# Kernel tuning notes

Measured on AMD Instinct MI355X. Metric: run time of the kernel, lower is better.

## Reference

```python
import jax, jax.numpy as jnp
import numpy as np

D = 1024
N_A = 4096
N_V = 4096


def setup_inputs() -> dict:
    key = jax.random.key(0)
    ks = jax.random.split(key, 6)
    s = 1.0 / np.sqrt(D)  # like torch Linear default init scale
    return {
        "inputs_a": jax.random.normal(ks[0], (N_A, D), dtype=jnp.float32),
        "inputs_v": jax.random.normal(ks[1], (N_V, D), dtype=jnp.float32),
        "W_Ba": jax.random.uniform(ks[2], (D, D), jnp.float32, -s, s),
        "W_Aa": jax.random.uniform(ks[3], (D, D), jnp.float32, -s, s),
        "W_Bv": jax.random.uniform(ks[4], (D, D), jnp.float32, -s, s),
        "W_Av": jax.random.uniform(ks[5], (D, D), jnp.float32, -s, s),
    }


def reference(inputs_a, inputs_v, W_Ba, W_Aa, W_Bv, W_Av):
    # torch Linear: y = x @ W.T ; weights stored [out, in]
    a_a = inputs_a @ W_Aa.T                      # [N_a, D]
    b_a = inputs_a @ W_Ba.T                      # [N_a, D]
    a_v = inputs_v @ W_Av.T                      # [N_v, D]
    b_v = inputs_v @ W_Bv.T                      # [N_v, D]
    scores = b_a @ a_v.T                         # [N_a, N_v]
    alpha_av = jax.nn.softmax(scores, axis=1)    # softmax over N_v
    att_avv = alpha_av @ b_v                     # [N_a, D]
    att_vaa = alpha_av.T @ a_a                   # [N_v, D]
    feature_map_a = att_avv + inputs_a
    feature_map_v = att_vaa + inputs_v
    return feature_map_a, feature_map_v
```

## Files before the change

### kernel.cpp

```cpp
#include <hip/hip_runtime.h>
#include <stdint.h>

#define D_DIM 1024
#define NA_DIM 4096
#define NV_DIM 4096

typedef __bf16 bf16_t;
typedef __bf16 bf16x8 __attribute__((ext_vector_type(8)));
typedef float f32x4 __attribute__((ext_vector_type(4)));

__device__ __forceinline__ void gload_lds16(const void* g, void* lds) {
  __builtin_amdgcn_global_load_lds(
      (const __attribute__((address_space(1))) unsigned int*)g,
      (__attribute__((address_space(3))) unsigned int*)lds, 16, 0, 0);
}

#define VMW(N) asm volatile("s_waitcnt vmcnt(" #N ")" ::: "memory")
#define LKW(N) asm volatile("s_waitcnt lgkmcnt(" #N ")" ::: "memory")
#define SB0() __builtin_amdgcn_sched_barrier(0)
#define BAR() asm volatile("s_barrier" ::: "memory")

__device__ __forceinline__ void gemm256_8ph(const bf16_t* __restrict__ A,
                                            const bf16_t* __restrict__ B,
                                            int K, int kb, int klen, int bm, int bn,
                                            bf16_t* lds, f32x4 acc[8][4]) {
  const int tid = threadIdx.x;
  const int lane = tid & 63;
  const int wid = tid >> 6;
  const int wm = wid >> 2;
  const int wn = wid & 3;
  const int frow = lane & 15;
  const int hi = lane >> 4;
  const int k0e = ((hi ^ (frow & 7)) << 3);

  const int sr = (wid << 4) + (lane >> 3);
  const int sc = (((lane & 7) ^ (lane >> 3)) << 3);
  const bf16_t* pAs = A + (size_t)(bm + sr) * K + kb + sc;
  const bf16_t* pBs = B + (size_t)(bn + sr) * K + kb + sc;
  const int dstW = wid << 10;

  const int aBase = (wm << 13) + frow * 64 + k0e;
  const int bBase = 16384 + ((wn >> 1) << 13) + ((wn & 1) << 12) + frow * 64 + k0e;

#define STG_A(kt, h, bufb) do { \
    const bf16_t* s_ = pAs + (size_t)((h) * 128) * K + (size_t)(kt) * 64; \
    bf16_t* d_ = lds + (bufb) * 32768 + (h) * 8192 + dstW; \
    gload_lds16(s_, d_); gload_lds16(s_ + (size_t)8 * K, d_ + 512); } while (0)
#define STG_B(kt, h, bufb) do { \
    const bf16_t* s_ = pBs + (size_t)((h) * 128) * K + (size_t)(kt) * 64; \
    bf16_t* d_ = lds + (bufb) * 32768 + 16384 + (h) * 8192 + dstW; \
    gload_lds16(s_, d_); gload_lds16(s_ + (size_t)8 * K, d_ + 512); } while (0)

  bf16x8 aF[2][4];
  bf16x8 bF[2][4][2];

#define READ_A(S, BUFB, Q) do { const bf16_t* Lb_ = lds + (BUFB) * 32768; \
    aF[S][0] = *(const bf16x8*)&Lb_[aBase + (Q) * 2048]; \
    aF[S][1] = *(const bf16x8*)&Lb_[(aBase ^ 32) + (Q) * 2048]; \
    aF[S][2] = *(const bf16x8*)&Lb_[aBase + (Q) * 2048 + 1024]; \
    aF[S][3] = *(const bf16x8*)&Lb_[(aBase ^ 32) + (Q) * 2048 + 1024]; } while (0)
#define READ_B(S, BUFB) do { const bf16_t* Lb_ = lds + (BUFB) * 32768; \
    _Pragma("unroll") for (int fc = 0; fc < 4; ++fc) { \
      bF[S][fc][0] = *(const bf16x8*)&Lb_[bBase + fc * 1024]; \
      bF[S][fc][1] = *(const bf16x8*)&Lb_[(bBase ^ 32) + fc * 1024]; } } while (0)

#define MFMA16(AS, BS, Q) do { \
    __builtin_amdgcn_s_setprio(1); \
    _Pragma("unroll") for (int fc = 0; fc < 4; ++fc) { \
      acc[(Q) * 2][fc]     = __builtin_amdgcn_mfma_f32_16x16x32_bf16(aF[AS][0], bF[BS][fc][0], acc[(Q) * 2][fc], 0, 0, 0); \
      acc[(Q) * 2][fc]     = __builtin_amdgcn_mfma_f32_16x16x32_bf16(aF[AS][1], bF[BS][fc][1], acc[(Q) * 2][fc], 0, 0, 0); \
      acc[(Q) * 2 + 1][fc] = __builtin_amdgcn_mfma_f32_16x16x32_bf16(aF[AS][2], bF[BS][fc][0], acc[(Q) * 2 + 1][fc], 0, 0, 0); \
      acc[(Q) * 2 + 1][fc] = __builtin_amdgcn_mfma_f32_16x16x32_bf16(aF[AS][3], bF[BS][fc][1], acc[(Q) * 2 + 1][fc], 0, 0, 0); \
    } \
    __builtin_amdgcn_s_setprio(0); } while (0)

  const int NI = klen >> 7;

  STG_B(0, 0, 0); STG_B(0, 1, 0); STG_A(0, 0, 0); STG_A(0, 1, 0);
  STG_B(1, 0, 1); STG_B(1, 1, 1);
  VMW(4);
  BAR();
  READ_B(0, 0); READ_A(0, 0, 0);

  for (int it = 0; it < NI; ++it) {
    const int T = 2 * it;
    const bool more = (it + 1 < NI);
    BAR(); STG_A(T + 1, 0, 1); READ_A(1, 0, 1); LKW(4); SB0(); MFMA16(0, 0, 0);
    BAR(); STG_A(T + 1, 1, 1); READ_A(0, 0, 2); LKW(4); SB0(); MFMA16(1, 0, 1);
    BAR(); if (more) STG_B(T + 2, 0, 0); READ_A(1, 0, 3); LKW(4); SB0(); MFMA16(0, 0, 2);
    BAR(); if (more) { STG_B(T + 2, 1, 0); VMW(4); } else { VMW(0); }
    READ_B(1, 1); READ_A(0, 1, 0); LKW(12); SB0(); MFMA16(1, 0, 3);
    BAR(); if (more) STG_A(T + 2, 0, 0); READ_A(1, 1, 1); LKW(4); SB0(); MFMA16(0, 1, 0);
    BAR(); if (more) STG_A(T + 2, 1, 0); READ_A(0, 1, 2); LKW(4); SB0(); MFMA16(1, 1, 1);
    BAR(); if (more) STG_B(T + 3, 0, 1); READ_A(1, 1, 3); LKW(4); SB0(); MFMA16(0, 1, 2);
    BAR();
    if (more) { STG_B(T + 3, 1, 1); VMW(4); READ_B(0, 0); READ_A(0, 0, 0); LKW(12); }
    else { LKW(0); }
    SB0(); MFMA16(1, 1, 3);
  }
#undef MFMA16
#undef READ_A
#undef READ_B
#undef STG_A
#undef STG_B
}

template <int BF16OUT>
__device__ __forceinline__ void store256(void* Cv, int ldc, int bm, int bn, f32x4 acc[8][4]) {
  const int lane = threadIdx.x & 63;
  const int wid = threadIdx.x >> 6;
  const int wm = wid >> 2, wn = wid & 3;
  const int frow = lane & 15, hi = lane >> 4;
  const int row0 = bm + wm * 128 + hi * 4;
  const int col0 = bn + wn * 64 + frow;
#pragma unroll
  for (int rf = 0; rf < 8; ++rf)
#pragma unroll
    for (int fc = 0; fc < 4; ++fc)
#pragma unroll
      for (int r = 0; r < 4; ++r) {
        size_t idx = (size_t)(row0 + rf * 16 + r) * ldc + (col0 + fc * 16);
        if constexpr (BF16OUT) ((bf16_t*)Cv)[idx] = (bf16_t)acc[rf][fc][r];
        else ((float*)Cv)[idx] = acc[rf][fc][r];
      }
}

__global__ __launch_bounds__(512, 2) void gemm_proj4(
    const bf16_t* __restrict__ Xa, const bf16_t* __restrict__ Xv,
    const bf16_t* __restrict__ W0, const bf16_t* __restrict__ W1,
    const bf16_t* __restrict__ W2, const bf16_t* __restrict__ W3,
    bf16_t* __restrict__ C0, bf16_t* __restrict__ C1,
    bf16_t* __restrict__ C2, bf16_t* __restrict__ C3) {
  __shared__ bf16_t lds[65536];
  const int z = blockIdx.z;
  const bf16_t* A = (z < 2) ? Xa : Xv;
  const bf16_t* B = (z == 0) ? W0 : (z == 1) ? W1 : (z == 2) ? W2 : W3;
  bf16_t* C = (z == 0) ? C0 : (z == 1) ? C1 : (z == 2) ? C2 : C3;
  f32x4 acc[8][4] = {};
  gemm256_8ph(A, B, D_DIM, 0, D_DIM, blockIdx.x * 256, blockIdx.y * 256, lds, acc);
  store256<1>(C, D_DIM, blockIdx.x * 256, blockIdx.y * 256, acc);
}

__global__ __launch_bounds__(512, 2) void gemm_scores(const bf16_t* __restrict__ A,
                                                      const bf16_t* __restrict__ B,
                                                      float* __restrict__ C) {
  __shared__ bf16_t lds[65536];
  f32x4 acc[8][4] = {};
  gemm256_8ph(A, B, D_DIM, 0, D_DIM, blockIdx.x * 256, blockIdx.y * 256, lds, acc);
  store256<0>(C, NV_DIM, blockIdx.x * 256, blockIdx.y * 256, acc);
}

__global__ __launch_bounds__(512, 2) void gemm_splitk(
    const bf16_t* __restrict__ alpha, const bf16_t* __restrict__ bvT,
    const bf16_t* __restrict__ alphaT, const bf16_t* __restrict__ aaT,
    float* __restrict__ P) {
  __shared__ bf16_t lds[65536];
  const int z = blockIdx.z;
  const bf16_t* A = (z < 2) ? alpha : alphaT;
  const bf16_t* B = (z < 2) ? bvT : aaT;
  const int kb = (z & 1) * 2048;
  f32x4 acc[8][4] = {};
  gemm256_8ph(A, B, 4096, kb, 2048, blockIdx.x * 256, blockIdx.y * 256, lds, acc);
  store256<0>(P + (size_t)z * NA_DIM * D_DIM, D_DIM, blockIdx.x * 256, blockIdx.y * 256, acc);
}

__global__ __launch_bounds__(256) void reduce_splitk(const float* __restrict__ P,
                                                     const float* __restrict__ resA,
                                                     const float* __restrict__ resV,
                                                     float* __restrict__ out) {
  const int g = blockIdx.y;
  const size_t n = (size_t)NA_DIM * D_DIM;
  size_t i = ((size_t)blockIdx.x * 256 + threadIdx.x) * 4;
  const float* p0 = P + (size_t)g * 2 * n;
  const float* p1 = p0 + n;
  const float* r = g ? resV : resA;
  float4 a = *(const float4*)(p0 + i);
  float4 b = *(const float4*)(p1 + i);
  float4 c = *(const float4*)(r + i);
  float4 o = {a.x + b.x + c.x, a.y + b.y + c.y, a.z + b.z + c.z, a.w + b.w + c.w};
  *(float4*)(out + g * n + i) = o;
}

__device__ __forceinline__ void cvt8(const float* in, bf16_t* out, int i) {
  float4 v0 = *(const float4*)(in + i);
  float4 v1 = *(const float4*)(in + i + 4);
  bf16x8 o;
  o[0] = (bf16_t)v0.x; o[1] = (bf16_t)v0.y; o[2] = (bf16_t)v0.z; o[3] = (bf16_t)v0.w;
  o[4] = (bf16_t)v1.x; o[5] = (bf16_t)v1.y; o[6] = (bf16_t)v1.z; o[7] = (bf16_t)v1.w;
  *(bf16x8*)(out + i) = o;
}

__global__ __launch_bounds__(256) void cvt2(const float* __restrict__ inA,
                                            const float* __restrict__ inV,
                                            bf16_t* __restrict__ oA,
                                            bf16_t* __restrict__ oV) {
  const float* in = blockIdx.y ? inV : inA;
  bf16_t* out = blockIdx.y ? oV : oA;
  cvt8(in, out, (blockIdx.x * 256 + threadIdx.x) * 8);
}

__global__ __launch_bounds__(256) void cvt4(const float* __restrict__ i0, const float* __restrict__ i1,
                                            const float* __restrict__ i2, const float* __restrict__ i3,
                                            bf16_t* __restrict__ o0, bf16_t* __restrict__ o1,
                                            bf16_t* __restrict__ o2, bf16_t* __restrict__ o3) {
  const int z = blockIdx.y;
  const float* in = (z == 0) ? i0 : (z == 1) ? i1 : (z == 2) ? i2 : i3;
  bf16_t* out = (z == 0) ? o0 : (z == 1) ? o1 : (z == 2) ? o2 : o3;
  cvt8(in, out, (blockIdx.x * 256 + threadIdx.x) * 8);
}

__global__ __launch_bounds__(256) void softmax_rows(const float* __restrict__ S,
                                                    bf16_t* __restrict__ P) {
  const int row = blockIdx.x;
  const int ncol = 4096;
  const float* s = S + (size_t)row * ncol;
  const int base = threadIdx.x * 16;
  float v[16];
  float4* vp = (float4*)v;
#pragma unroll
  for (int q = 0; q < 4; ++q) vp[q] = *(const float4*)(s + base + q * 4);
  float m = v[0];
#pragma unroll
  for (int q = 1; q < 16; ++q) m = fmaxf(m, v[q]);
  for (int off = 32; off; off >>= 1) m = fmaxf(m, __shfl_xor(m, off));
  __shared__ float sm[4], ss[4];
  const int wid = threadIdx.x >> 6, lane = threadIdx.x & 63;
  if (lane == 0) sm[wid] = m;
  __syncthreads();
  m = fmaxf(fmaxf(sm[0], sm[1]), fmaxf(sm[2], sm[3]));
  float sum = 0.f;
#pragma unroll
  for (int q = 0; q < 16; ++q) { v[q] = __expf(v[q] - m); sum += v[q]; }
  for (int off = 32; off; off >>= 1) sum += __shfl_xor(sum, off);
  if (lane == 0) ss[wid] = sum;
  __syncthreads();
  const float inv = 1.0f / (ss[0] + ss[1] + ss[2] + ss[3]);
  bf16x8 o0, o1;
#pragma unroll
  for (int q = 0; q < 8; ++q) { o0[q] = (bf16_t)(v[q] * inv); o1[q] = (bf16_t)(v[q + 8] * inv); }
  bf16_t* p = P + (size_t)row * ncol + base;
  *(bf16x8*)p = o0;
  *(bf16x8*)(p + 8) = o1;
}

__global__ __launch_bounds__(256) void transpose_bf16(const bf16_t* __restrict__ in,
                                                      bf16_t* __restrict__ out, int R, int C) {
  __shared__ bf16_t t[64][72];
  const int bx = blockIdx.x * 64;
  const int by = blockIdx.y * 64;
  const int tid = threadIdx.x;
  const int c8 = (tid & 7) * 8;
  const int r = tid >> 3;
#pragma unroll
  for (int rr = 0; rr < 64; rr += 32) {
    bf16x8 v = *(const bf16x8*)(in + (size_t)(by + r + rr) * C + bx + c8);
    *(bf16x8*)&t[r + rr][c8] = v;
  }
  __syncthreads();
#pragma unroll
  for (int rr = 0; rr < 64; rr += 32) {
    bf16x8 v;
#pragma unroll
    for (int q = 0; q < 8; ++q) v[q] = t[c8 + q][r + rr];
    *(bf16x8*)(out + (size_t)(bx + r + rr) * R + by + c8) = v;
  }
}

extern "C" void kernel_launch(void* const* d_in, const int* in_sizes, int n_in,
                              void* d_out, int out_size, void* d_ws, size_t ws_size,
                              hipStream_t stream) {
  (void)in_sizes; (void)n_in; (void)out_size; (void)ws_size;
  const float* inA = (const float*)d_in[0];
  const float* inV = (const float*)d_in[1];
  const float* wBa = (const float*)d_in[2];
  const float* wAa = (const float*)d_in[3];
  const float* wBv = (const float*)d_in[4];
  const float* wAv = (const float*)d_in[5];
  float* out = (float*)d_out;

  char* w = (char*)d_ws;
  auto take = [&](size_t bytes) { void* p = (void*)w; w += bytes; return p; };
  const size_t XB = (size_t)NA_DIM * D_DIM * 2;
  const size_t WB = (size_t)D_DIM * D_DIM * 2;
  bf16_t* XaB = (bf16_t*)take(XB);
  bf16_t* XvB = (bf16_t*)take(XB);
  bf16_t* WBaB = (bf16_t*)take(WB);
  bf16_t* WAaB = (bf16_t*)take(WB);
  bf16_t* WBvB = (bf16_t*)take(WB);
  bf16_t* WAvB = (bf16_t*)take(WB);
  bf16_t* b_a = (bf16_t*)take(XB);
  bf16_t* a_v = (bf16_t*)take(XB);
  bf16_t* a_a = (bf16_t*)take(XB);
  bf16_t* b_v = (bf16_t*)take(XB);
  bf16_t* a_aT = (bf16_t*)take(XB);
  bf16_t* b_vT = (bf16_t*)take(XB);
  float* scores = (float*)take((size_t)NA_DIM * NV_DIM * 4);
  bf16_t* alpha = (bf16_t*)take((size_t)NA_DIM * NV_DIM * 2);
  bf16_t* alphaT = (bf16_t*)take((size_t)NA_DIM * NV_DIM * 2);
  float* P = scores;

  cvt2<<<dim3(NA_DIM * D_DIM / 2048, 2), 256, 0, stream>>>(inA, inV, XaB, XvB);
  cvt4<<<dim3(D_DIM * D_DIM / 2048, 4), 256, 0, stream>>>(wBa, wAa, wAv, wBv,
                                                          WBaB, WAaB, WAvB, WBvB);

  gemm_proj4<<<dim3(NA_DIM / 256, D_DIM / 256, 4), 512, 0, stream>>>(
      XaB, XvB, WBaB, WAaB, WAvB, WBvB, b_a, a_a, a_v, b_v);

  gemm_scores<<<dim3(NA_DIM / 256, NV_DIM / 256), 512, 0, stream>>>(b_a, a_v, scores);

  softmax_rows<<<NA_DIM, 256, 0, stream>>>(scores, alpha);

  transpose_bf16<<<dim3(NV_DIM / 64, NA_DIM / 64), 256, 0, stream>>>(alpha, alphaT, NA_DIM, NV_DIM);
  transpose_bf16<<<dim3(D_DIM / 64, NA_DIM / 64), 256, 0, stream>>>(a_a, a_aT, NA_DIM, D_DIM);
  transpose_bf16<<<dim3(D_DIM / 64, NV_DIM / 64), 256, 0, stream>>>(b_v, b_vT, NV_DIM, D_DIM);

  gemm_splitk<<<dim3(NA_DIM / 256, D_DIM / 256, 4), 512, 0, stream>>>(
      alpha, b_vT, alphaT, a_aT, P);
  reduce_splitk<<<dim3(NA_DIM * D_DIM / 1024, 2), 256, 0, stream>>>(P, inA, inV, out);
}
```

Measured before the change: 224.6 us.

## Replace double-buffered register fragment pipeline with single-buffer LDS read-then-compute tiles

Rewrites the GEMM main loop so each phase loads its A/B fragments from LDS, waits for all LDS reads (lgkmcnt 0), and then issues its MFMAs, adding extra barriers around each phase. The old ping-pong register fragments, which let the LDS reads for the next phase overlap the current MFMAs, are removed. This lowers register pressure and simplifies the schedule, at the cost of exposing LDS read latency and adding more barrier stalls.

```diff
diff --git a/kernel.cpp b/kernel.cpp
--- a/kernel.cpp
+++ b/kernel.cpp
@@ -51,53 +51,60 @@
     bf16_t* d_ = lds + (bufb) * 32768 + 16384 + (h) * 8192 + dstW; \
     gload_lds16(s_, d_); gload_lds16(s_ + (size_t)8 * K, d_ + 512); } while (0)
 
-  bf16x8 aF[2][4];
-  bf16x8 bF[2][4][2];
-
-#define READ_A(S, BUFB, Q) do { const bf16_t* Lb_ = lds + (BUFB) * 32768; \
-    aF[S][0] = *(const bf16x8*)&Lb_[aBase + (Q) * 2048]; \
-    aF[S][1] = *(const bf16x8*)&Lb_[(aBase ^ 32) + (Q) * 2048]; \
-    aF[S][2] = *(const bf16x8*)&Lb_[aBase + (Q) * 2048 + 1024]; \
-    aF[S][3] = *(const bf16x8*)&Lb_[(aBase ^ 32) + (Q) * 2048 + 1024]; } while (0)
-#define READ_B(S, BUFB) do { const bf16_t* Lb_ = lds + (BUFB) * 32768; \
+  bf16x8 aF[4];
+  bf16x8 bF[4][2];
+
+#define READ_A(Q, BUFB) do { const bf16_t* Lb_ = lds + (BUFB) * 32768; \
+    aF[0] = *(const bf16x8*)&Lb_[aBase + (Q) * 2048]; \
+    aF[1] = *(const bf16x8*)&Lb_[(aBase ^ 32) + (Q) * 2048]; \
+    aF[2] = *(const bf16x8*)&Lb_[aBase + (Q) * 2048 + 1024]; \
+    aF[3] = *(const bf16x8*)&Lb_[(aBase ^ 32) + (Q) * 2048 + 1024]; } while (0)
+#define READ_B(BUFB) do { const bf16_t* Lb_ = lds + (BUFB) * 32768; \
     _Pragma("unroll") for (int fc = 0; fc < 4; ++fc) { \
-      bF[S][fc][0] = *(const bf16x8*)&Lb_[bBase + fc * 1024]; \
-      bF[S][fc][1] = *(const bf16x8*)&Lb_[(bBase ^ 32) + fc * 1024]; } } while (0)
-
-#define MFMA16(AS, BS, Q) do { \
+      bF[fc][0] = *(const bf16x8*)&Lb_[bBase + fc * 1024]; \
+      bF[fc][1] = *(const bf16x8*)&Lb_[(bBase ^ 32) + fc * 1024]; } } while (0)
+
+#define MFMA16(Q) do { \
     __builtin_amdgcn_s_setprio(1); \
     _Pragma("unroll") for (int fc = 0; fc < 4; ++fc) { \
-      acc[(Q) * 2][fc]     = __builtin_amdgcn_mfma_f32_16x16x32_bf16(aF[AS][0], bF[BS][fc][0], acc[(Q) * 2][fc], 0, 0, 0); \
-      acc[(Q) * 2][fc]     = __builtin_amdgcn_mfma_f32_16x16x32_bf16(aF[AS][1], bF[BS][fc][1], acc[(Q) * 2][fc], 0, 0, 0); \
-      acc[(Q) * 2 + 1][fc] = __builtin_amdgcn_mfma_f32_16x16x32_bf16(aF[AS][2], bF[BS][fc][0], acc[(Q) * 2 + 1][fc], 0, 0, 0); \
-      acc[(Q) * 2 + 1][fc] = __builtin_amdgcn_mfma_f32_16x16x32_bf16(aF[AS][3], bF[BS][fc][1], acc[(Q) * 2 + 1][fc], 0, 0, 0); \
+      acc[(Q) * 2][fc]     = __builtin_amdgcn_mfma_f32_16x16x32_bf16(aF[0], bF[fc][0], acc[(Q) * 2][fc], 0, 0, 0); \
+      acc[(Q) * 2][fc]     = __builtin_amdgcn_mfma_f32_16x16x32_bf16(aF[1], bF[fc][1], acc[(Q) * 2][fc], 0, 0, 0); \
+      acc[(Q) * 2 + 1][fc] = __builtin_amdgcn_mfma_f32_16x16x32_bf16(aF[2], bF[fc][0], acc[(Q) * 2 + 1][fc], 0, 0, 0); \
+      acc[(Q) * 2 + 1][fc] = __builtin_amdgcn_mfma_f32_16x16x32_bf16(aF[3], bF[fc][1], acc[(Q) * 2 + 1][fc], 0, 0, 0); \
     } \
     __builtin_amdgcn_s_setprio(0); } while (0)
 
-  const int NI = klen >> 7;
+#define TILE(P, T) do { \
+    const bool mA = ((T) + 1 < NT); \
+    const bool mB = ((T) + 2 < NT); \
+     \
+    READ_B(P); READ_A(0, P); if (mA) STG_A((T) + 1, 0, (P) ^ 1); \
+    BAR(); LKW(0); SB0(); MFMA16(0); BAR(); \
+     \
+    READ_A(1, P); if (mA) STG_A((T) + 1, 1, (P) ^ 1); \
+    BAR(); LKW(0); SB0(); MFMA16(1); BAR(); \
+     \
+    READ_A(2, P); if (mB) STG_B((T) + 2, 0, P); \
+    BAR(); LKW(0); SB0(); MFMA16(2); BAR(); \
+     \
+    READ_A(3, P); if (mB) STG_B((T) + 2, 1, P); \
+    if (mB) { VMW(4); } else { VMW(0); } \
+    BAR(); LKW(0); SB0(); MFMA16(3); BAR(); \
+  } while (0)
+
+  const int NT = klen >> 6;
 
   STG_B(0, 0, 0); STG_B(0, 1, 0); STG_A(0, 0, 0); STG_A(0, 1, 0);
   STG_B(1, 0, 1); STG_B(1, 1, 1);
   VMW(4);
   BAR();
-  READ_B(0, 0); READ_A(0, 0, 0);
-
-  for (int it = 0; it < NI; ++it) {
-    const int T = 2 * it;
-    const bool more = (it + 1 < NI);
-    BAR(); STG_A(T + 1, 0, 1); READ_A(1, 0, 1); LKW(4); SB0(); MFMA16(0, 0, 0);
-    BAR(); STG_A(T + 1, 1, 1); READ_A(0, 0, 2); LKW(4); SB0(); MFMA16(1, 0, 1);
-    BAR(); if (more) STG_B(T + 2, 0, 0); READ_A(1, 0, 3); LKW(4); SB0(); MFMA16(0, 0, 2);
-    BAR(); if (more) { STG_B(T + 2, 1, 0); VMW(4); } else { VMW(0); }
-    READ_B(1, 1); READ_A(0, 1, 0); LKW(12); SB0(); MFMA16(1, 0, 3);
-    BAR(); if (more) STG_A(T + 2, 0, 0); READ_A(1, 1, 1); LKW(4); SB0(); MFMA16(0, 1, 0);
-    BAR(); if (more) STG_A(T + 2, 1, 0); READ_A(0, 1, 2); LKW(4); SB0(); MFMA16(1, 1, 1);
-    BAR(); if (more) STG_B(T + 3, 0, 1); READ_A(1, 1, 3); LKW(4); SB0(); MFMA16(0, 1, 2);
-    BAR();
-    if (more) { STG_B(T + 3, 1, 1); VMW(4); READ_B(0, 0); READ_A(0, 0, 0); LKW(12); }
-    else { LKW(0); }
-    SB0(); MFMA16(1, 1, 3);
+
+  for (int it = 0; it < (NT >> 1); ++it) {
+    TILE(0, 2 * it);
+    TILE(1, 2 * it + 1);
   }
+  VMW(0);
+#undef TILE
 #undef MFMA16
 #undef READ_A
 #undef READ_B
```

After: 210.6 us. 1.07x faster.
